# Performance work log

Measured on AMD Instinct MI355X. Metric: run time of the kernel, lower is better.

The kernel has to match this reference:

```python
import jax, jax.numpy as jnp
import numpy as np

B, T, C, F = 512, 1024, 8, 8
ISIZE = C * F  # 64
OSIZE = 64


def setup_inputs() -> dict:
    key = jax.random.key(0)
    k_x, k_w, k_b = jax.random.split(key, 3)
    x = jax.random.normal(k_x, (B, T, C, F), dtype=jnp.float32)
    # per-group Linear params, torch nn.Linear layout: weight [osize, isize], bias [osize]
    bound = 1.0 / np.sqrt(ISIZE)
    W = jax.random.uniform(k_w, (T, OSIZE, ISIZE), dtype=jnp.float32, minval=-bound, maxval=bound)
    b = jax.random.uniform(k_b, (T, OSIZE), dtype=jnp.float32, minval=-bound, maxval=bound)
    return {"x": x, "W": W, "b": b}


def reference(x, W, b):
    # collapseDims: cat(x.split(1, 2), 3).squeeze(2) == reshape [B,T,C,F] -> [B,T,C*F]
    Bn, Tn, Cn, Fn = x.shape
    xc = x.reshape(Bn, Tn, Cn * Fn)
    # per-slice Linear along dim=1 (T groups): y[b,t,:] = xc[b,t,:] @ W[t].T + b[t]
    out = jnp.einsum("bti,toi->bto", xc, W) + b[None, :, :]
    return out
```

## Files before the change

kernel.cpp:

```cpp
#include <hip/hip_runtime.h>


#define T_DIM 1024
#define B_DIM 512
#define KSZ 64
#define OSZ 64
#define ROWS 64

__global__ __launch_bounds__(256, 5) void pl_kernel(
    const float* __restrict__ x,
    const float* __restrict__ W,
    const float* __restrict__ bias,
    float* __restrict__ out)
{
    __shared__ float Wt[KSZ * OSZ];
    __shared__ float Xs[KSZ * ROWS];

    const int t     = blockIdx.x >> 3;
    const int chunk = blockIdx.x & 7;
    const int row0  = chunk * ROWS;
    const int tid   = threadIdx.x;

    {
        const int o  = tid & 63;
        const int ib = (tid >> 6) << 4;
        const float* wg = W + (size_t)t * (OSZ * KSZ) + (size_t)o * KSZ + ib;
        #pragma unroll
        for (int c = 0; c < 4; ++c) {
            float4 wv = *(const float4*)(wg + 4 * c);
            Wt[(ib + 4 * c + 0) * OSZ + o] = wv.x;
            Wt[(ib + 4 * c + 1) * OSZ + o] = wv.y;
            Wt[(ib + 4 * c + 2) * OSZ + o] = wv.z;
            Wt[(ib + 4 * c + 3) * OSZ + o] = wv.w;
        }
    }

    {
        const int g = tid >> 4;
        const int q = tid & 15;
        const float* xg = x + ((size_t)(row0 + 4 * g) * T_DIM + t) * KSZ + 4 * q;
        float4 a0 = *(const float4*)(xg);
        float4 a1 = *(const float4*)(xg + (size_t)T_DIM * KSZ);
        float4 a2 = *(const float4*)(xg + 2 * (size_t)T_DIM * KSZ);
        float4 a3 = *(const float4*)(xg + 3 * (size_t)T_DIM * KSZ);
        float4 v0 = make_float4(a0.x, a1.x, a2.x, a3.x);
        float4 v1 = make_float4(a0.y, a1.y, a2.y, a3.y);
        float4 v2 = make_float4(a0.z, a1.z, a2.z, a3.z);
        float4 v3 = make_float4(a0.w, a1.w, a2.w, a3.w);
        const int p = (g ^ q) << 2;
        *(float4*)&Xs[(4 * q + 0) * ROWS + p] = v0;
        *(float4*)&Xs[(4 * q + 1) * ROWS + p] = v1;
        *(float4*)&Xs[(4 * q + 2) * ROWS + p] = v2;
        *(float4*)&Xs[(4 * q + 3) * ROWS + p] = v3;
    }

    __syncthreads();

    const int tr = tid >> 4;
    const int tc = tid & 15;

    float acc[4][4] = {};

    #pragma unroll 8
    for (int i = 0; i < KSZ; ++i) {
        const int f = i >> 2;
        float4 xv = *(const float4*)&Xs[i * ROWS + ((tr ^ f) << 2)];
        float4 wv = *(const float4*)&Wt[i * OSZ + (tc << 2)];
        acc[0][0] += xv.x * wv.x; acc[0][1] += xv.x * wv.y; acc[0][2] += xv.x * wv.z; acc[0][3] += xv.x * wv.w;
        acc[1][0] += xv.y * wv.x; acc[1][1] += xv.y * wv.y; acc[1][2] += xv.y * wv.z; acc[1][3] += xv.y * wv.w;
        acc[2][0] += xv.z * wv.x; acc[2][1] += xv.z * wv.y; acc[2][2] += xv.z * wv.z; acc[2][3] += xv.z * wv.w;
        acc[3][0] += xv.w * wv.x; acc[3][1] += xv.w * wv.y; acc[3][2] += xv.w * wv.z; acc[3][3] += xv.w * wv.w;
    }

    float4 bv = *(const float4*)(bias + (size_t)t * OSZ + (tc << 2));
    #pragma unroll
    for (int k = 0; k < 4; ++k) {
        int b = row0 + tr * 4 + k;
        float4 res;
        res.x = acc[k][0] + bv.x;
        res.y = acc[k][1] + bv.y;
        res.z = acc[k][2] + bv.z;
        res.w = acc[k][3] + bv.w;
        *(float4*)(out + ((size_t)b * T_DIM + t) * OSZ + (tc << 2)) = res;
    }
}

extern "C" void kernel_launch(void* const* d_in, const int* in_sizes, int n_in,
                              void* d_out, int out_size, void* d_ws, size_t ws_size,
                              hipStream_t stream) {
    const float* x    = (const float*)d_in[0];
    const float* W    = (const float*)d_in[1];
    const float* bias = (const float*)d_in[2];
    float* out        = (float*)d_out;

    dim3 grid(T_DIM * (B_DIM / ROWS));
    dim3 block(256);
    pl_kernel<<<grid, block, 0, stream>>>(x, W, bias, out);
}
```

Measured before the change: 78.77 us.

## Loop each block over all batch chunks with register prefetch of next X tile

Each block now handles one time step t and iterates over all 8 batch chunks, so the W tile is loaded and transposed once per t instead of eight times. The next X chunk is prefetched into registers while the current chunk is computed, and a sync protects the shared X buffer between chunks. The grid shrinks from 8192 to 1024 blocks and launch bounds drop to 4 waves per SIMD. This lowers parallelism and adds serial dependence per block, which can hurt latency hiding in a memory-bound kernel.

```diff
diff --git a/kernel.cpp b/kernel.cpp
--- a/kernel.cpp
+++ b/kernel.cpp
@@ -6,8 +6,9 @@
 #define KSZ 64
 #define OSZ 64
 #define ROWS 64
+#define NCHUNK (B_DIM / ROWS)
 
-__global__ __launch_bounds__(256, 5) void pl_kernel(
+__global__ __launch_bounds__(256, 4) void pl_kernel(
     const float* __restrict__ x,
     const float* __restrict__ W,
     const float* __restrict__ bias,
@@ -16,72 +17,88 @@
     __shared__ float Wt[KSZ * OSZ];
     __shared__ float Xs[KSZ * ROWS];
 
-    const int t     = blockIdx.x >> 3;
-    const int chunk = blockIdx.x & 7;
-    const int row0  = chunk * ROWS;
-    const int tid   = threadIdx.x;
+    const int t   = blockIdx.x;
+    const int tid = threadIdx.x;
 
     {
         const int o  = tid & 63;
         const int ib = (tid >> 6) << 4;
         const float* wg = W + (size_t)t * (OSZ * KSZ) + (size_t)o * KSZ + ib;
         #pragma unroll
-        for (int c = 0; c < 4; ++c) {
-            float4 wv = *(const float4*)(wg + 4 * c);
-            Wt[(ib + 4 * c + 0) * OSZ + o] = wv.x;
-            Wt[(ib + 4 * c + 1) * OSZ + o] = wv.y;
-            Wt[(ib + 4 * c + 2) * OSZ + o] = wv.z;
-            Wt[(ib + 4 * c + 3) * OSZ + o] = wv.w;
+        for (int cc = 0; cc < 4; ++cc) {
+            float4 wv = *(const float4*)(wg + 4 * cc);
+            Wt[(ib + 4 * cc + 0) * OSZ + o] = wv.x;
+            Wt[(ib + 4 * cc + 1) * OSZ + o] = wv.y;
+            Wt[(ib + 4 * cc + 2) * OSZ + o] = wv.z;
+            Wt[(ib + 4 * cc + 3) * OSZ + o] = wv.w;
         }
     }
 
+    const int g = tid >> 4;
+    const int q = tid & 15;
+
+    const size_t rstride = (size_t)T_DIM * KSZ;
+    const size_t cstride = (size_t)ROWS * rstride;
+    const float* xg0 = x + ((size_t)(4 * g) * T_DIM + t) * KSZ + 4 * q;
+
+    float4 a0, a1, a2, a3;
     {
-        const int g = tid >> 4;
-        const int q = tid & 15;
-        const float* xg = x + ((size_t)(row0 + 4 * g) * T_DIM + t) * KSZ + 4 * q;
-        float4 a0 = *(const float4*)(xg);
-        float4 a1 = *(const float4*)(xg + (size_t)T_DIM * KSZ);
-        float4 a2 = *(const float4*)(xg + 2 * (size_t)T_DIM * KSZ);
-        float4 a3 = *(const float4*)(xg + 3 * (size_t)T_DIM * KSZ);
+        const float* p = xg0;
+        a0 = *(const float4*)(p);
+        a1 = *(const float4*)(p + rstride);
+        a2 = *(const float4*)(p + 2 * rstride);
+        a3 = *(const float4*)(p + 3 * rstride);
+    }
+
+    const float4 bv = *(const float4*)(bias + (size_t)t * OSZ + (q << 2));
+
+    for (int c = 0; c < NCHUNK; ++c) {
         float4 v0 = make_float4(a0.x, a1.x, a2.x, a3.x);
         float4 v1 = make_float4(a0.y, a1.y, a2.y, a3.y);
         float4 v2 = make_float4(a0.z, a1.z, a2.z, a3.z);
         float4 v3 = make_float4(a0.w, a1.w, a2.w, a3.w);
+
+        if (c > 0) __syncthreads();
+
         const int p = (g ^ q) << 2;
         *(float4*)&Xs[(4 * q + 0) * ROWS + p] = v0;
         *(float4*)&Xs[(4 * q + 1) * ROWS + p] = v1;
         *(float4*)&Xs[(4 * q + 2) * ROWS + p] = v2;
         *(float4*)&Xs[(4 * q + 3) * ROWS + p] = v3;
-    }
 
-    __syncthreads();
+        if (c + 1 < NCHUNK) {
+            const float* pn = xg0 + (size_t)(c + 1) * cstride;
+            a0 = *(const float4*)(pn);
+            a1 = *(const float4*)(pn + rstride);
+            a2 = *(const float4*)(pn + 2 * rstride);
+            a3 = *(const float4*)(pn + 3 * rstride);
+        }
 
-    const int tr = tid >> 4;
-    const int tc = tid & 15;
+        __syncthreads();
 
-    float acc[4][4] = {};
+        float acc[4][4] = {};
+        #pragma unroll 8
+        for (int i = 0; i < KSZ; ++i) {
+            const int f = i >> 2;
+            float4 xv = *(const float4*)&Xs[i * ROWS + ((g ^ f) << 2)];
+            float4 wv = *(const float4*)&Wt[i * OSZ + (q << 2)];
+            acc[0][0] += xv.x * wv.x; acc[0][1] += xv.x * wv.y; acc[0][2] += xv.x * wv.z; acc[0][3] += xv.x * wv.w;
+            acc[1][0] += xv.y * wv.x; acc[1][1] += xv.y * wv.y; acc[1][2] += xv.y * wv.z; acc[1][3] += xv.y * wv.w;
+            acc[2][0] += xv.z * wv.x; acc[2][1] += xv.z * wv.y; acc[2][2] += xv.z * wv.z; acc[2][3] += xv.z * wv.w;
+            acc[3][0] += xv.w * wv.x; acc[3][1] += xv.w * wv.y; acc[3][2] += xv.w * wv.z; acc[3][3] += xv.w * wv.w;
+        }
 
-    #pragma unroll 8
-    for (int i = 0; i < KSZ; ++i) {
-        const int f = i >> 2;
-        float4 xv = *(const float4*)&Xs[i * ROWS + ((tr ^ f) << 2)];
-        float4 wv = *(const float4*)&Wt[i * OSZ + (tc << 2)];
-        acc[0][0] += xv.x * wv.x; acc[0][1] += xv.x * wv.y; acc[0][2] += xv.x * wv.z; acc[0][3] += xv.x * wv.w;
-        acc[1][0] += xv.y * wv.x; acc[1][1] += xv.y * wv.y; acc[1][2] += xv.y * wv.z; acc[1][3] += xv.y * wv.w;
-        acc[2][0] += xv.z * wv.x; acc[2][1] += xv.z * wv.y; acc[2][2] += xv.z * wv.z; acc[2][3] += xv.z * wv.w;
-        acc[3][0] += xv.w * wv.x; acc[3][1] += xv.w * wv.y; acc[3][2] += xv.w * wv.z; acc[3][3] += xv.w * wv.w;
-    }
-
-    float4 bv = *(const float4*)(bias + (size_t)t * OSZ + (tc << 2));
-    #pragma unroll
-    for (int k = 0; k < 4; ++k) {
-        int b = row0 + tr * 4 + k;
-        float4 res;
-        res.x = acc[k][0] + bv.x;
-        res.y = acc[k][1] + bv.y;
-        res.z = acc[k][2] + bv.z;
-        res.w = acc[k][3] + bv.w;
-        *(float4*)(out + ((size_t)b * T_DIM + t) * OSZ + (tc << 2)) = res;
+        const int row0 = c * ROWS;
+        #pragma unroll
+        for (int k = 0; k < 4; ++k) {
+            const int b = row0 + g * 4 + k;
+            float4 res;
+            res.x = acc[k][0] + bv.x;
+            res.y = acc[k][1] + bv.y;
+            res.z = acc[k][2] + bv.z;
+            res.w = acc[k][3] + bv.w;
+            *(float4*)(out + ((size_t)b * T_DIM + t) * OSZ + (q << 2)) = res;
+        }
     }
 }
 
@@ -93,7 +110,7 @@
     const float* bias = (const float*)d_in[2];
     float* out        = (float*)d_out;
 
-    dim3 grid(T_DIM * (B_DIM / ROWS));
+    dim3 grid(T_DIM);
     dim3 block(256);
     pl_kernel<<<grid, block, 0, stream>>>(x, W, bias, out);
 }
```

After: 75.92 us. -3.6%, faster.
